# Optimization experiments

Measured on AMD Instinct MI355X. Metric: run time of the kernel, lower is better.

The kernel has to match this reference:

```python
import jax, jax.numpy as jnp
import numpy as np

N_NODES = 1_000_000
N_EDGES = 16_000_000
F_IN, F_H1, F_H2, N_CLS = 32, 16, 8, 5
N_GRAPHS = 10_000


def setup_inputs() -> dict:
    key = jax.random.key(0)
    ks = jax.random.split(key, 10)
    x = jax.random.normal(ks[0], (N_NODES, F_IN), dtype=jnp.float32)
    edge_index = jax.random.randint(ks[1], (2, N_EDGES), 0, N_NODES, dtype=jnp.int32)
    batch = jnp.sort(jax.random.randint(ks[2], (N_NODES,), 0, N_GRAPHS, dtype=jnp.int32))
    # learned params (Glorot-ish scale)
    W1 = jax.random.normal(ks[3], (F_IN, F_H1), dtype=jnp.float32) / np.sqrt(F_IN)
    b1 = jnp.zeros((F_H1,), dtype=jnp.float32)
    W2 = jax.random.normal(ks[4], (F_H1, F_H2), dtype=jnp.float32) / np.sqrt(F_H1)
    b2 = jnp.zeros((F_H2,), dtype=jnp.float32)
    Wl = jax.random.normal(ks[5], (F_H2, N_CLS), dtype=jnp.float32) / np.sqrt(F_H2)
    bl = jnp.zeros((N_CLS,), dtype=jnp.float32)
    return {"x": x, "edge_index": edge_index, "batch": batch, "num_graphs": N_GRAPHS,
            "W1": W1, "b1": b1, "W2": W2, "b2": b2, "Wl": Wl, "bl": bl}


def _gcn_conv(x, W, b, src, dst, deg_inv_sqrt, norm_e, num_nodes):
    # h = X W, then symmetric-normalized aggregation with self loops:
    # out_i = sum_{(j->i)} norm_ji * h_j + deg_i^{-1} * h_i + b
    h = x @ W                                  # [N, F_out]
    msg = h[src] * norm_e[:, None]             # [E, F_out] gather + scale
    agg = jax.ops.segment_sum(msg, dst, num_segments=num_nodes)
    self_loop = h * (deg_inv_sqrt * deg_inv_sqrt)[:, None]
    return agg + self_loop + b


def reference(x, edge_index, batch, num_graphs, W1, b1, W2, b2, Wl, bl):
    num_nodes = x.shape[0]
    src, dst = edge_index[0], edge_index[1]
    # degrees including self loops (GCN: A_hat = A + I)
    deg = jax.ops.segment_sum(jnp.ones_like(dst, dtype=x.dtype), dst,
                              num_segments=num_nodes) + 1.0
    deg_inv_sqrt = jax.lax.rsqrt(deg)
    norm_e = deg_inv_sqrt[src] * deg_inv_sqrt[dst]   # [E]

    h = _gcn_conv(x, W1, b1, src, dst, deg_inv_sqrt, norm_e, num_nodes)
    h = jax.nn.relu(h)
    h = _gcn_conv(h, W2, b2, src, dst, deg_inv_sqrt, norm_e, num_nodes)
    h = jax.nn.relu(h)

    # global_mean_pool over graph ids
    sums = jax.ops.segment_sum(h, batch, num_segments=num_graphs)     # [G, F_H2]
    cnts = jax.ops.segment_sum(jnp.ones((num_nodes,), dtype=h.dtype), batch,
                               num_segments=num_graphs)
    pooled = sums / jnp.maximum(cnts, 1.0)[:, None]
    return pooled @ Wl + bl
```

## Files before the change

### kernel.cpp

```cpp
#include <hip/hip_runtime.h>


namespace {

constexpr int F_IN = 32, F_H1 = 16, F_H2 = 8, N_CLS = 5;
constexpr int BB = 9, NPB = 1 << BB;
constexpr int MAXB = 2048;
constexpr int CHUNK = 8192;

typedef float v4f __attribute__((ext_vector_type(4)));


__global__ void k_mm1(const float* __restrict__ x, const float* __restrict__ W,
                      const float* __restrict__ dis, float* __restrict__ hp, int N) {
  __shared__ float w[F_IN * F_H1];
  for (int k = threadIdx.x; k < F_IN * F_H1; k += blockDim.x) w[k] = W[k];
  __syncthreads();
  int i = blockIdx.x * blockDim.x + threadIdx.x;
  if (i >= N) return;
  const v4f* xr = reinterpret_cast<const v4f*>(x + (size_t)i * F_IN);
  float acc[F_H1];
#pragma unroll
  for (int f = 0; f < F_H1; ++f) acc[f] = 0.f;
#pragma unroll
  for (int k4 = 0; k4 < F_IN / 4; ++k4) {
    v4f v = __builtin_nontemporal_load(&xr[k4]);
    float vv[4] = {v.x, v.y, v.z, v.w};
#pragma unroll
    for (int j = 0; j < 4; ++j) {
      const float* wr = &w[(k4 * 4 + j) * F_H1];
#pragma unroll
      for (int f = 0; f < F_H1; ++f) acc[f] = fmaf(vv[j], wr[f], acc[f]);
    }
  }
  float di = dis ? dis[i] : 1.f;
  v4f* hr = reinterpret_cast<v4f*>(hp + (size_t)i * F_H1);
#pragma unroll
  for (int q = 0; q < F_H1 / 4; ++q) {
    v4f r;
    r.x = di * acc[q * 4];
    r.y = di * acc[q * 4 + 1];
    r.z = di * acc[q * 4 + 2];
    r.w = di * acc[q * 4 + 3];
    hr[q] = r;
  }
}

__global__ void k_mm2(const float* __restrict__ in, const float* __restrict__ W,
                      const float* __restrict__ dis, float* __restrict__ hp, int N) {
  __shared__ float w[F_H1 * F_H2];
  for (int k = threadIdx.x; k < F_H1 * F_H2; k += blockDim.x) w[k] = W[k];
  __syncthreads();
  int i = blockIdx.x * blockDim.x + threadIdx.x;
  if (i >= N) return;
  const v4f* xr = reinterpret_cast<const v4f*>(in + (size_t)i * F_H1);
  float acc[F_H2];
#pragma unroll
  for (int f = 0; f < F_H2; ++f) acc[f] = 0.f;
#pragma unroll
  for (int k4 = 0; k4 < F_H1 / 4; ++k4) {
    v4f v = __builtin_nontemporal_load(&xr[k4]);
    float vv[4] = {v.x, v.y, v.z, v.w};
#pragma unroll
    for (int j = 0; j < 4; ++j) {
      const float* wr = &w[(k4 * 4 + j) * F_H2];
#pragma unroll
      for (int f = 0; f < F_H2; ++f) acc[f] = fmaf(vv[j], wr[f], acc[f]);
    }
  }
  float di = dis ? dis[i] : 1.f;
  v4f* hr = reinterpret_cast<v4f*>(hp + (size_t)i * F_H2);
#pragma unroll
  for (int q = 0; q < F_H2 / 4; ++q) {
    v4f r;
    r.x = di * acc[q * 4];
    r.y = di * acc[q * 4 + 1];
    r.z = di * acc[q * 4 + 2];
    r.w = di * acc[q * 4 + 3];
    hr[q] = r;
  }
}

__global__ void k_final(const float* __restrict__ pooled, const float* __restrict__ cnts,
                        const float* __restrict__ Wl, const float* __restrict__ bl,
                        float* __restrict__ out, int total) {
  int gid = blockIdx.x * blockDim.x + threadIdx.x;
  if (gid >= total) return;
  int g = gid / N_CLS, c = gid % N_CLS;
  float s = 0.f;
#pragma unroll
  for (int f = 0; f < F_H2; ++f) s += pooled[g * F_H2 + f] * Wl[f * N_CLS + c];
  out[gid] = s / fmaxf(cnts[g], 1.f) + bl[c];
}


__global__ void k_hist(const int* __restrict__ dst, int* __restrict__ bcnt,
                       int E, int nbuck) {
  __shared__ int h[MAXB];
  for (int i = threadIdx.x; i < MAXB; i += blockDim.x) h[i] = 0;
  __syncthreads();
  for (int e = blockIdx.x * blockDim.x + threadIdx.x; e < E;
       e += gridDim.x * blockDim.x)
    atomicAdd(&h[__builtin_nontemporal_load(&dst[e]) >> BB], 1);
  __syncthreads();
  for (int i = threadIdx.x; i < nbuck; i += blockDim.x)
    if (h[i]) atomicAdd(&bcnt[i], h[i]);
}

__global__ void k_bscan(const int* __restrict__ bcnt, int* __restrict__ bbase,
                        int* __restrict__ bcur, int nbuck, int E) {
  __shared__ int stmp[1024];
  int t = threadIdx.x;
  int i0 = t * 2;
  int v0 = (i0 < nbuck) ? bcnt[i0] : 0;
  int v1 = (i0 + 1 < nbuck) ? bcnt[i0 + 1] : 0;
  int sum = v0 + v1;
  stmp[t] = sum;
  __syncthreads();
  for (int off = 1; off < 1024; off <<= 1) {
    int x = (t >= off) ? stmp[t - off] : 0;
    __syncthreads();
    stmp[t] += x;
    __syncthreads();
  }
  int run = stmp[t] - sum;
  if (i0 < nbuck) { bbase[i0] = run; bcur[i0] = run; }
  if (i0 + 1 < nbuck) { bbase[i0 + 1] = run + v0; bcur[i0 + 1] = run + v0; }
  if (t == 0) bbase[nbuck] = E;
}

__global__ __launch_bounds__(256)
void k_binscatter(const int* __restrict__ dst, const int* __restrict__ src,
                  int* __restrict__ bcur, int* __restrict__ packed, int E) {
  __shared__ int hist[MAXB];
  __shared__ int sbase[MAXB];
  __shared__ int lcur[MAXB];
  __shared__ int stg[CHUNK];
  __shared__ int stmp[256];
  int t = threadIdx.x;
  int c0 = blockIdx.x * CHUNK;
  int n = min(CHUNK, E - c0);
  for (int i = t; i < MAXB; i += 256) hist[i] = 0;
  __syncthreads();
  for (int j = t; j < n; j += 256)
    atomicAdd(&hist[__builtin_nontemporal_load(&dst[c0 + j]) >> BB], 1);
  __syncthreads();
  int v[8], sum = 0;
  int b8 = t * 8;
#pragma unroll
  for (int k = 0; k < 8; ++k) { v[k] = hist[b8 + k]; sum += v[k]; }
  stmp[t] = sum;
  __syncthreads();
  for (int off = 1; off < 256; off <<= 1) {
    int x = (t >= off) ? stmp[t - off] : 0;
    __syncthreads();
    stmp[t] += x;
    __syncthreads();
  }
  int run = stmp[t] - sum;
#pragma unroll
  for (int k = 0; k < 8; ++k) { sbase[b8 + k] = run; lcur[b8 + k] = run; run += v[k]; }
  __syncthreads();
  for (int i = t; i < MAXB; i += 256) {
    int c = hist[i];
    if (c) hist[i] = atomicAdd(&bcur[i], c);
  }
  __syncthreads();
  for (int j = t; j < n; j += 256) {
    int d = __builtin_nontemporal_load(&dst[c0 + j]);
    int s = __builtin_nontemporal_load(&src[c0 + j]);
    int b = d >> BB;
    int p = atomicAdd(&lcur[b], 1);
    stg[p] = ((d & (NPB - 1)) << 20) | s;
  }
  __syncthreads();
  for (int j = t; j < n; j += 256) {
    int lo = 0, hi = MAXB - 1;
    while (lo < hi) {
      int mid = (lo + hi + 1) >> 1;
      if (sbase[mid] <= j) lo = mid; else hi = mid - 1;
    }
    packed[hist[lo] + (j - sbase[lo])] = stg[j];
  }
}

__global__ void k_dis_b(const int* __restrict__ bbase, const int* __restrict__ packed,
                        float* __restrict__ dis, int N) {
  __shared__ int cnt[NPB];
  int t = threadIdx.x;
  for (int i = t; i < NPB; i += blockDim.x) cnt[i] = 0;
  __syncthreads();
  int b = blockIdx.x;
  int beg = bbase[b], end = bbase[b + 1];
  for (int e = beg + t; e < end; e += blockDim.x)
    atomicAdd(&cnt[__builtin_nontemporal_load(&packed[e]) >> 20], 1);
  __syncthreads();
  int node0 = b << BB;
  for (int i = t; i < NPB; i += blockDim.x) {
    int node = node0 + i;
    if (node < N) dis[node] = rsqrtf((float)cnt[i] + 1.0f);
  }
}


template <int F>
__global__ __launch_bounds__(512, 8)
void k_conv(const int* __restrict__ bbase, const int* __restrict__ packed,
            const float* __restrict__ dis, const float* __restrict__ hp,
            const float* __restrict__ bias, float* __restrict__ out, int N) {
  __shared__ float acc[NPB * F];
  int t = threadIdx.x;
  int b = blockIdx.x;
  int node0 = b << BB;
  for (int i4 = t; i4 < NPB * F / 4; i4 += 512) {
    int idx = i4 * 4;
    int node = node0 + idx / F;
    v4f v = {0.f, 0.f, 0.f, 0.f};
    if (node < N) v = *reinterpret_cast<const v4f*>(hp + (size_t)node0 * F + idx);
    *reinterpret_cast<v4f*>(&acc[idx]) = v;
  }
  __syncthreads();
  int beg = bbase[b], end = bbase[b + 1];
  const int EPI = 512 / F;
  int f = t % F, eg = t / F;
  for (int e = beg + eg; e < end; e += 4 * EPI) {
    int pe[4]; float hv[4]; int dl[4]; bool ok[4];
#pragma unroll
    for (int u = 0; u < 4; ++u) {
      int ee = e + u * EPI;
      ok[u] = ee < end;
      pe[u] = ok[u] ? __builtin_nontemporal_load(&packed[ee]) : 0;
    }
#pragma unroll
    for (int u = 0; u < 4; ++u) {
      int s = pe[u] & 0xFFFFF;
      dl[u] = pe[u] >> 20;
      hv[u] = ok[u] ? hp[(size_t)s * F + f] : 0.f;
    }
#pragma unroll
    for (int u = 0; u < 4; ++u)
      if (ok[u]) atomicAdd(&acc[dl[u] * F + f], hv[u]);
  }
  __syncthreads();
  for (int i4 = t; i4 < NPB * F / 4; i4 += 512) {
    int idx = i4 * 4;
    int node = node0 + idx / F;
    if (node >= N) continue;
    int ff = idx % F;
    float di = dis[node];
    v4f a = *reinterpret_cast<const v4f*>(&acc[idx]);
    v4f r;
    r.x = fmaxf(fmaf(di, a.x, bias[ff + 0]), 0.f);
    r.y = fmaxf(fmaf(di, a.y, bias[ff + 1]), 0.f);
    r.z = fmaxf(fmaf(di, a.z, bias[ff + 2]), 0.f);
    r.w = fmaxf(fmaf(di, a.w, bias[ff + 3]), 0.f);
    __builtin_nontemporal_store(r, reinterpret_cast<v4f*>(out + (size_t)node0 * F + idx));
  }
}

__global__ __launch_bounds__(512, 8)
void k_conv_pool(const int* __restrict__ bbase, const int* __restrict__ packed,
                 const float* __restrict__ dis, const float* __restrict__ hp,
                 const float* __restrict__ bias, const int* __restrict__ batch,
                 float* __restrict__ pooled, float* __restrict__ cnts, int N) {
  constexpr int F = F_H2;
  __shared__ float acc[NPB * F];
  int t = threadIdx.x;
  int b = blockIdx.x;
  int node0 = b << BB;
  for (int i4 = t; i4 < NPB * F / 4; i4 += 512) {
    int idx = i4 * 4;
    int node = node0 + idx / F;
    v4f v = {0.f, 0.f, 0.f, 0.f};
    if (node < N) v = *reinterpret_cast<const v4f*>(hp + (size_t)node0 * F + idx);
    *reinterpret_cast<v4f*>(&acc[idx]) = v;
  }
  __syncthreads();
  int beg = bbase[b], end = bbase[b + 1];
  const int EPI = 512 / F;
  int f = t % F, eg = t / F;
  for (int e = beg + eg; e < end; e += 4 * EPI) {
    int pe[4]; float hv[4]; int dl[4]; bool ok[4];
#pragma unroll
    for (int u = 0; u < 4; ++u) {
      int ee = e + u * EPI;
      ok[u] = ee < end;
      pe[u] = ok[u] ? __builtin_nontemporal_load(&packed[ee]) : 0;
    }
#pragma unroll
    for (int u = 0; u < 4; ++u) {
      int s = pe[u] & 0xFFFFF;
      dl[u] = pe[u] >> 20;
      hv[u] = ok[u] ? hp[(size_t)s * F + f] : 0.f;
    }
#pragma unroll
    for (int u = 0; u < 4; ++u)
      if (ok[u]) atomicAdd(&acc[dl[u] * F + f], hv[u]);
  }
  __syncthreads();
  for (int i = t; i < NPB * F; i += 512) {
    int node = node0 + i / F;
    if (node >= N) continue;
    int ff = i % F;
    float di = dis[node];
    float v = fmaxf(fmaf(di, acc[i], bias[ff]), 0.f);
    int g = batch[node];
    atomicAdd(&pooled[g * F_H2 + ff], v);
    if (ff == 0) atomicAdd(&cnts[g], 1.0f);
  }
}


__global__ void k_deg(const int* __restrict__ dst, float* __restrict__ deg, int E) {
  int e = blockIdx.x * blockDim.x + threadIdx.x;
  if (e < E) atomicAdd(&deg[dst[e]], 1.0f);
}
__global__ void k_dis(float* __restrict__ d, int N) {
  int i = blockIdx.x * blockDim.x + threadIdx.x;
  if (i < N) d[i] = rsqrtf(d[i] + 1.0f);
}
template <int F>
__global__ void k_edge(const int* __restrict__ src, const int* __restrict__ dst,
                       const float* __restrict__ dis, const float* __restrict__ h,
                       float* __restrict__ agg, int total) {
  int gid = blockIdx.x * blockDim.x + threadIdx.x;
  if (gid >= total) return;
  int e = gid / F, f = gid % F;
  int s = src[e], d = dst[e];
  atomicAdd(&agg[d * F + f], h[s * F + f] * dis[s] * dis[d]);
}
template <int F>
__global__ void k_combine(const float* __restrict__ h, const float* __restrict__ dis,
                          const float* __restrict__ b, float* __restrict__ agg, int total) {
  int gid = blockIdx.x * blockDim.x + threadIdx.x;
  if (gid >= total) return;
  int i = gid / F, f = gid % F;
  float di = dis[i];
  agg[gid] = fmaxf(agg[gid] + h[gid] * di * di + b[f], 0.f);
}
__global__ void k_combine_pool_fb(const float* __restrict__ h2, const float* __restrict__ agg2,
                                  const float* __restrict__ dis, const float* __restrict__ b,
                                  const int* __restrict__ batch, float* __restrict__ pooled,
                                  float* __restrict__ cnts, int total) {
  int gid = blockIdx.x * blockDim.x + threadIdx.x;
  if (gid >= total) return;
  int i = gid >> 3, f = gid & 7;
  float di = dis[i];
  float v = fmaxf(agg2[gid] + h2[gid] * di * di + b[f], 0.f);
  int g = batch[i];
  atomicAdd(&pooled[g * F_H2 + f], v);
  if (f == 0) atomicAdd(&cnts[g], 1.0f);
}

}

extern "C" void kernel_launch(void* const* d_in, const int* in_sizes, int n_in,
                              void* d_out, int out_size, void* d_ws, size_t ws_size,
                              hipStream_t stream) {
  const float* x   = (const float*)d_in[0];
  const int* ei    = (const int*)d_in[1];
  const int* batch = (const int*)d_in[2];
  const float* W1 = (const float*)d_in[4];
  const float* b1 = (const float*)d_in[5];
  const float* W2 = (const float*)d_in[6];
  const float* b2 = (const float*)d_in[7];
  const float* Wl = (const float*)d_in[8];
  const float* bl = (const float*)d_in[9];

  const int N = in_sizes[0] / F_IN;
  const int E = in_sizes[1] / 2;
  const int G = out_size / N_CLS;
  const int* src  = ei;
  const int* dstp = ei + E;

  const int BLK = 256;
  const int nbuck = (N + NPB - 1) >> BB;

  size_t need = (size_t)(3 * MAXB + 8) * 4
              + (size_t)E * 4
              + (size_t)N * 4
              + (size_t)N * F_H1 * 4
              + (size_t)N * F_H1 * 4
              + (size_t)G * (F_H2 + 1) * 4 + 1024;

  if (N <= (1 << 20) && nbuck <= MAXB && ws_size >= need) {
    char* p = (char*)d_ws;
    int*   bcnt   = (int*)p;    p += (size_t)MAXB * 4;
    int*   bbase  = (int*)p;    p += (size_t)(MAXB + 4) * 4;
    int*   bcur   = (int*)p;    p += (size_t)MAXB * 4;
    int*   packed = (int*)p;    p += (size_t)E * 4;
    float* dis    = (float*)p;  p += (size_t)N * 4;
    float* H      = (float*)p;  p += (size_t)N * F_H1 * 4;
    float* O      = (float*)p;  p += (size_t)N * F_H1 * 4;
    float* pooled = (float*)p;  p += (size_t)G * F_H2 * 4;
    float* cnts   = (float*)p;

    (void)hipMemsetAsync(bcnt, 0, (size_t)MAXB * 4, stream);
    (void)hipMemsetAsync(pooled, 0, ((size_t)G * F_H2 + G) * 4, stream);

    k_hist<<<2048, BLK, 0, stream>>>(dstp, bcnt, E, nbuck);
    k_bscan<<<1, 1024, 0, stream>>>(bcnt, bbase, bcur, nbuck, E);
    k_binscatter<<<(E + CHUNK - 1) / CHUNK, BLK, 0, stream>>>(dstp, src, bcur, packed, E);
    k_dis_b<<<nbuck, BLK, 0, stream>>>(bbase, packed, dis, N);

    k_mm1<<<(N + BLK - 1) / BLK, BLK, 0, stream>>>(x, W1, dis, H, N);
    k_conv<F_H1><<<nbuck, 512, 0, stream>>>(bbase, packed, dis, H, b1, O, N);
    k_mm2<<<(N + BLK - 1) / BLK, BLK, 0, stream>>>(O, W2, dis, H, N);
    k_conv_pool<<<nbuck, 512, 0, stream>>>(bbase, packed, dis, H, b2, batch,
                                           pooled, cnts, N);

    k_final<<<(G * N_CLS + BLK - 1) / BLK, BLK, 0, stream>>>(
        pooled, cnts, Wl, bl, (float*)d_out, G * N_CLS);
    return;
  }

  float* ws = (float*)d_ws;
  float* dis    = ws;
  float* A      = ws + N;
  float* B      = A + (size_t)N * F_H1;
  float* h2     = A;
  float* agg2   = A + (size_t)N * F_H2;
  float* pooled = B + (size_t)N * F_H1;
  float* cnts   = pooled + (size_t)G * F_H2;

  (void)hipMemsetAsync(dis, 0, (size_t)N * sizeof(float), stream);
  (void)hipMemsetAsync(B, 0, (size_t)N * F_H1 * sizeof(float), stream);
  (void)hipMemsetAsync(pooled, 0, ((size_t)G * F_H2 + G) * sizeof(float), stream);

  k_deg<<<(E + BLK - 1) / BLK, BLK, 0, stream>>>(dstp, dis, E);
  k_dis<<<(N + BLK - 1) / BLK, BLK, 0, stream>>>(dis, N);
  k_mm1<<<(N + BLK - 1) / BLK, BLK, 0, stream>>>(x, W1, nullptr, A, N);
  k_edge<F_H1><<<(E * F_H1 + BLK - 1) / BLK, BLK, 0, stream>>>(src, dstp, dis, A, B, E * F_H1);
  k_combine<F_H1><<<(N * F_H1 + BLK - 1) / BLK, BLK, 0, stream>>>(A, dis, b1, B, N * F_H1);
  (void)hipMemsetAsync(agg2, 0, (size_t)N * F_H2 * sizeof(float), stream);
  k_mm2<<<(N + BLK - 1) / BLK, BLK, 0, stream>>>(B, W2, nullptr, h2, N);
  k_edge<F_H2><<<(E * F_H2 + BLK - 1) / BLK, BLK, 0, stream>>>(src, dstp, dis, h2, agg2, E * F_H2);
  k_combine_pool_fb<<<(N * F_H2 + BLK - 1) / BLK, BLK, 0, stream>>>(
      h2, agg2, dis, b2, batch, pooled, cnts, N * F_H2);
  k_final<<<(G * N_CLS + BLK - 1) / BLK, BLK, 0, stream>>>(
      pooled, cnts, Wl, bl, (float*)d_out, G * N_CLS);
}
```

Before: 3.520 ms.

## Use larger dst buckets and vectorized float4 gathers in GCN conv kernels

Doubles the nodes per destination bucket (1024 buckets of 1024 nodes) and enlarges the binscatter chunk, adjusting the scans to match. The conv kernels now have each thread gather a float4 of source features per edge instead of a single float. The shared accumulator is switched to a feature-major layout, and the unroll depth rises to 8 edges in flight. The aim is fewer, wider gather transactions and more memory-level parallelism. The costs are more LDS per block (64KB for F=16), lower occupancy with the min-blocks hint removed, and four LDS atomics per thread per edge.

```diff
diff --git a/kernel.cpp b/kernel.cpp
--- a/kernel.cpp
+++ b/kernel.cpp
@@ -4,9 +4,9 @@
 namespace {
 
 constexpr int F_IN = 32, F_H1 = 16, F_H2 = 8, N_CLS = 5;
-constexpr int BB = 9, NPB = 1 << BB;
-constexpr int MAXB = 2048;
-constexpr int CHUNK = 8192;
+constexpr int BB = 10, NPB = 1 << BB;
+constexpr int MAXB = 1024;
+constexpr int CHUNK = 12288;
 
 typedef float v4f __attribute__((ext_vector_type(4)));
 
@@ -109,23 +109,19 @@
 
 __global__ void k_bscan(const int* __restrict__ bcnt, int* __restrict__ bbase,
                         int* __restrict__ bcur, int nbuck, int E) {
-  __shared__ int stmp[1024];
+  __shared__ int s[MAXB];
   int t = threadIdx.x;
-  int i0 = t * 2;
-  int v0 = (i0 < nbuck) ? bcnt[i0] : 0;
-  int v1 = (i0 + 1 < nbuck) ? bcnt[i0 + 1] : 0;
-  int sum = v0 + v1;
-  stmp[t] = sum;
-  __syncthreads();
-  for (int off = 1; off < 1024; off <<= 1) {
-    int x = (t >= off) ? stmp[t - off] : 0;
+  int v = (t < nbuck) ? bcnt[t] : 0;
+  s[t] = v;
+  __syncthreads();
+  for (int off = 1; off < MAXB; off <<= 1) {
+    int x = (t >= off) ? s[t - off] : 0;
     __syncthreads();
-    stmp[t] += x;
+    s[t] += x;
     __syncthreads();
   }
-  int run = stmp[t] - sum;
-  if (i0 < nbuck) { bbase[i0] = run; bcur[i0] = run; }
-  if (i0 + 1 < nbuck) { bbase[i0 + 1] = run + v0; bcur[i0 + 1] = run + v0; }
+  int ex = s[t] - v;
+  if (t < nbuck) { bbase[t] = ex; bcur[t] = ex; }
   if (t == 0) bbase[nbuck] = E;
 }
 
@@ -145,10 +141,10 @@
   for (int j = t; j < n; j += 256)
     atomicAdd(&hist[__builtin_nontemporal_load(&dst[c0 + j]) >> BB], 1);
   __syncthreads();
-  int v[8], sum = 0;
-  int b8 = t * 8;
-#pragma unroll
-  for (int k = 0; k < 8; ++k) { v[k] = hist[b8 + k]; sum += v[k]; }
+  int v[4], sum = 0;
+  int b4 = t * 4;
+#pragma unroll
+  for (int k = 0; k < 4; ++k) { v[k] = hist[b4 + k]; sum += v[k]; }
   stmp[t] = sum;
   __syncthreads();
   for (int off = 1; off < 256; off <<= 1) {
@@ -159,7 +155,7 @@
   }
   int run = stmp[t] - sum;
 #pragma unroll
-  for (int k = 0; k < 8; ++k) { sbase[b8 + k] = run; lcur[b8 + k] = run; run += v[k]; }
+  for (int k = 0; k < 4; ++k) { sbase[b4 + k] = run; lcur[b4 + k] = run; run += v[k]; }
   __syncthreads();
   for (int i = t; i < MAXB; i += 256) {
     int c = hist[i];
@@ -203,110 +199,130 @@
 }
 
 
-template <int F>
-__global__ __launch_bounds__(512, 8)
+template <int F, int U>
+__global__ __launch_bounds__(512)
 void k_conv(const int* __restrict__ bbase, const int* __restrict__ packed,
             const float* __restrict__ dis, const float* __restrict__ hp,
             const float* __restrict__ bias, float* __restrict__ out, int N) {
-  __shared__ float acc[NPB * F];
+  constexpr int RPE = F / 4;
+  constexpr int EPI = 512 / RPE;
+  __shared__ float acc[F * NPB];
   int t = threadIdx.x;
   int b = blockIdx.x;
   int node0 = b << BB;
-  for (int i4 = t; i4 < NPB * F / 4; i4 += 512) {
-    int idx = i4 * 4;
-    int node = node0 + idx / F;
+  for (int idx = t; idx < NPB * RPE; idx += 512) {
+    int node = idx / RPE, f4 = idx % RPE;
     v4f v = {0.f, 0.f, 0.f, 0.f};
-    if (node < N) v = *reinterpret_cast<const v4f*>(hp + (size_t)node0 * F + idx);
-    *reinterpret_cast<v4f*>(&acc[idx]) = v;
+    if (node0 + node < N)
+      v = *reinterpret_cast<const v4f*>(hp + (size_t)node0 * F + (size_t)idx * 4);
+#pragma unroll
+    for (int k = 0; k < 4; ++k) acc[(f4 * 4 + k) * NPB + node] = v[k];
   }
   __syncthreads();
   int beg = bbase[b], end = bbase[b + 1];
-  const int EPI = 512 / F;
-  int f = t % F, eg = t / F;
-  for (int e = beg + eg; e < end; e += 4 * EPI) {
-    int pe[4]; float hv[4]; int dl[4]; bool ok[4];
-#pragma unroll
-    for (int u = 0; u < 4; ++u) {
+  int f4 = t % RPE, eg = t / RPE;
+  int fb = f4 * 4;
+  for (int e = beg + eg; e < end; e += U * EPI) {
+    int pe[U]; bool ok[U];
+#pragma unroll
+    for (int u = 0; u < U; ++u) {
       int ee = e + u * EPI;
       ok[u] = ee < end;
-      pe[u] = ok[u] ? __builtin_nontemporal_load(&packed[ee]) : 0;
-    }
-#pragma unroll
-    for (int u = 0; u < 4; ++u) {
+      pe[u] = __builtin_nontemporal_load(&packed[ok[u] ? ee : beg]);
+    }
+    v4f hv[U];
+#pragma unroll
+    for (int u = 0; u < U; ++u) {
       int s = pe[u] & 0xFFFFF;
-      dl[u] = pe[u] >> 20;
-      hv[u] = ok[u] ? hp[(size_t)s * F + f] : 0.f;
-    }
-#pragma unroll
-    for (int u = 0; u < 4; ++u)
-      if (ok[u]) atomicAdd(&acc[dl[u] * F + f], hv[u]);
-  }
-  __syncthreads();
-  for (int i4 = t; i4 < NPB * F / 4; i4 += 512) {
-    int idx = i4 * 4;
-    int node = node0 + idx / F;
-    if (node >= N) continue;
-    int ff = idx % F;
-    float di = dis[node];
-    v4f a = *reinterpret_cast<const v4f*>(&acc[idx]);
+      hv[u] = *reinterpret_cast<const v4f*>(hp + (size_t)s * F + fb);
+    }
+#pragma unroll
+    for (int u = 0; u < U; ++u) {
+      int dl = pe[u] >> 20;
+      if (ok[u]) {
+#pragma unroll
+        for (int k = 0; k < 4; ++k)
+          atomicAdd(&acc[(fb + k) * NPB + dl], hv[u][k]);
+      }
+    }
+  }
+  __syncthreads();
+  for (int idx = t; idx < NPB * RPE; idx += 512) {
+    int node = idx / RPE, f4o = idx % RPE;
+    int g = node0 + node;
+    if (g >= N) continue;
+    float di = dis[g];
     v4f r;
-    r.x = fmaxf(fmaf(di, a.x, bias[ff + 0]), 0.f);
-    r.y = fmaxf(fmaf(di, a.y, bias[ff + 1]), 0.f);
-    r.z = fmaxf(fmaf(di, a.z, bias[ff + 2]), 0.f);
-    r.w = fmaxf(fmaf(di, a.w, bias[ff + 3]), 0.f);
-    __builtin_nontemporal_store(r, reinterpret_cast<v4f*>(out + (size_t)node0 * F + idx));
-  }
-}
-
-__global__ __launch_bounds__(512, 8)
+#pragma unroll
+    for (int k = 0; k < 4; ++k)
+      r[k] = fmaxf(fmaf(di, acc[(f4o * 4 + k) * NPB + node], bias[f4o * 4 + k]), 0.f);
+    __builtin_nontemporal_store(
+        r, reinterpret_cast<v4f*>(out + (size_t)node0 * F + (size_t)idx * 4));
+  }
+}
+
+template <int U>
+__global__ __launch_bounds__(512)
 void k_conv_pool(const int* __restrict__ bbase, const int* __restrict__ packed,
                  const float* __restrict__ dis, const float* __restrict__ hp,
                  const float* __restrict__ bias, const int* __restrict__ batch,
                  float* __restrict__ pooled, float* __restrict__ cnts, int N) {
   constexpr int F = F_H2;
-  __shared__ float acc[NPB * F];
+  constexpr int RPE = F / 4;
+  constexpr int EPI = 512 / RPE;
+  __shared__ float acc[F * NPB];
   int t = threadIdx.x;
   int b = blockIdx.x;
   int node0 = b << BB;
-  for (int i4 = t; i4 < NPB * F / 4; i4 += 512) {
-    int idx = i4 * 4;
-    int node = node0 + idx / F;
+  for (int idx = t; idx < NPB * RPE; idx += 512) {
+    int node = idx / RPE, f4 = idx % RPE;
     v4f v = {0.f, 0.f, 0.f, 0.f};
-    if (node < N) v = *reinterpret_cast<const v4f*>(hp + (size_t)node0 * F + idx);
-    *reinterpret_cast<v4f*>(&acc[idx]) = v;
+    if (node0 + node < N)
+      v = *reinterpret_cast<const v4f*>(hp + (size_t)node0 * F + (size_t)idx * 4);
+#pragma unroll
+    for (int k = 0; k < 4; ++k) acc[(f4 * 4 + k) * NPB + node] = v[k];
   }
   __syncthreads();
   int beg = bbase[b], end = bbase[b + 1];
-  const int EPI = 512 / F;
-  int f = t % F, eg = t / F;
-  for (int e = beg + eg; e < end; e += 4 * EPI) {
-    int pe[4]; float hv[4]; int dl[4]; bool ok[4];
-#pragma unroll
-    for (int u = 0; u < 4; ++u) {
+  int f4 = t % RPE, eg = t / RPE;
+  int fb = f4 * 4;
+  for (int e = beg + eg; e < end; e += U * EPI) {
+    int pe[U]; bool ok[U];
+#pragma unroll
+    for (int u = 0; u < U; ++u) {
       int ee = e + u * EPI;
       ok[u] = ee < end;
-      pe[u] = ok[u] ? __builtin_nontemporal_load(&packed[ee]) : 0;
-    }
-#pragma unroll
-    for (int u = 0; u < 4; ++u) {
+      pe[u] = __builtin_nontemporal_load(&packed[ok[u] ? ee : beg]);
+    }
+    v4f hv[U];
+#pragma unroll
+    for (int u = 0; u < U; ++u) {
       int s = pe[u] & 0xFFFFF;
-      dl[u] = pe[u] >> 20;
-      hv[u] = ok[u] ? hp[(size_t)s * F + f] : 0.f;
-    }
-#pragma unroll
-    for (int u = 0; u < 4; ++u)
-      if (ok[u]) atomicAdd(&acc[dl[u] * F + f], hv[u]);
-  }
-  __syncthreads();
-  for (int i = t; i < NPB * F; i += 512) {
-    int node = node0 + i / F;
-    if (node >= N) continue;
-    int ff = i % F;
-    float di = dis[node];
-    float v = fmaxf(fmaf(di, acc[i], bias[ff]), 0.f);
-    int g = batch[node];
-    atomicAdd(&pooled[g * F_H2 + ff], v);
-    if (ff == 0) atomicAdd(&cnts[g], 1.0f);
+      hv[u] = *reinterpret_cast<const v4f*>(hp + (size_t)s * F + fb);
+    }
+#pragma unroll
+    for (int u = 0; u < U; ++u) {
+      int dl = pe[u] >> 20;
+      if (ok[u]) {
+#pragma unroll
+        for (int k = 0; k < 4; ++k)
+          atomicAdd(&acc[(fb + k) * NPB + dl], hv[u][k]);
+      }
+    }
+  }
+  __syncthreads();
+  for (int idx = t; idx < NPB * RPE; idx += 512) {
+    int node = idx / RPE, f4o = idx % RPE;
+    int gn = node0 + node;
+    if (gn >= N) continue;
+    float di = dis[gn];
+    int g = batch[gn];
+#pragma unroll
+    for (int k = 0; k < 4; ++k) {
+      float v = fmaxf(fmaf(di, acc[(f4o * 4 + k) * NPB + node], bias[f4o * 4 + k]), 0.f);
+      atomicAdd(&pooled[g * F_H2 + f4o * 4 + k], v);
+    }
+    if (f4o == 0) atomicAdd(&cnts[g], 1.0f);
   }
 }
 
@@ -399,15 +415,15 @@
     (void)hipMemsetAsync(pooled, 0, ((size_t)G * F_H2 + G) * 4, stream);
 
     k_hist<<<2048, BLK, 0, stream>>>(dstp, bcnt, E, nbuck);
-    k_bscan<<<1, 1024, 0, stream>>>(bcnt, bbase, bcur, nbuck, E);
+    k_bscan<<<1, MAXB, 0, stream>>>(bcnt, bbase, bcur, nbuck, E);
     k_binscatter<<<(E + CHUNK - 1) / CHUNK, BLK, 0, stream>>>(dstp, src, bcur, packed, E);
     k_dis_b<<<nbuck, BLK, 0, stream>>>(bbase, packed, dis, N);
 
     k_mm1<<<(N + BLK - 1) / BLK, BLK, 0, stream>>>(x, W1, dis, H, N);
-    k_conv<F_H1><<<nbuck, 512, 0, stream>>>(bbase, packed, dis, H, b1, O, N);
+    k_conv<F_H1, 8><<<nbuck, 512, 0, stream>>>(bbase, packed, dis, H, b1, O, N);
     k_mm2<<<(N + BLK - 1) / BLK, BLK, 0, stream>>>(O, W2, dis, H, N);
-    k_conv_pool<<<nbuck, 512, 0, stream>>>(bbase, packed, dis, H, b2, batch,
-                                           pooled, cnts, N);
+    k_conv_pool<8><<<nbuck, 512, 0, stream>>>(bbase, packed, dis, H, b2, batch,
+                                              pooled, cnts, N);
 
     k_final<<<(G * N_CLS + BLK - 1) / BLK, BLK, 0, stream>>>(
         pooled, cnts, Wl, bl, (float*)d_out, G * N_CLS);
```

After: 3.745 ms. 1.06x slower.
